# Optimization experiments

Measured on AMD Instinct MI355X. Metric: run time of the kernel, lower is better.

## Reference

```python
import jax, jax.numpy as jnp
import numpy as np

S, B, D = 2048, 4, 512
H, R, QK, FFN = 8, 8, 32, 2048
HD = D // H  # 64


def _ln(x, g, b, eps=1e-5):
    mu = jnp.mean(x, axis=-1, keepdims=True)
    var = jnp.var(x, axis=-1, keepdims=True)
    return (x - mu) * jax.lax.rsqrt(var + eps) * g + b


def setup_inputs() -> dict:
    key = jax.random.key(0)
    ks = jax.random.split(key, 16)
    w = lambda k, shape: (jax.random.normal(k, shape, jnp.float32) * 0.02)
    return {
        "x": jax.random.normal(ks[0], (S, B, D), jnp.float32),
        "Wq": w(ks[1], (D, D)),        "bq": jnp.zeros((D,), jnp.float32),
        "Wk": w(ks[2], (D, D)),        "bk": jnp.zeros((D,), jnp.float32),
        "Wv": w(ks[3], (D, HD * R)),   "bv": jnp.zeros((HD * R,), jnp.float32),
        "Wqv": w(ks[4], (D, QK * H)),  "bqv": jnp.zeros((QK * H,), jnp.float32),
        "Wkv": w(ks[5], (HD, QK)),     "bkv": jnp.zeros((QK,), jnp.float32),
        "Wf": w(ks[6], (D, D)),        "bf": jnp.zeros((D,), jnp.float32),
        "W1": w(ks[7], (D, FFN)),      "b1": jnp.zeros((FFN,), jnp.float32),
        "W2": w(ks[8], (FFN, D)),      "b2": jnp.zeros((D,), jnp.float32),
        "g1": jnp.ones((D,), jnp.float32),  "be1": jnp.zeros((D,), jnp.float32),
        "g2": jnp.ones((D,), jnp.float32),  "be2": jnp.zeros((D,), jnp.float32),
    }


def reference(x, Wq, bq, Wk, bk, Wv, bv, Wqv, bqv, Wkv, bkv, Wf, bf,
              W1, b1, W2, b2, g1, be1, g2, be2):
    # x: [S, B, D] -> [B, S, D]
    xb = jnp.transpose(x, (1, 0, 2))
    bsz, n, _ = xb.shape
    res = xb

    # stage 1: per-head attention over positions
    q = (xb @ Wq + bq).reshape(bsz, n, H, HD) / np.sqrt(HD).astype(np.float32)
    k = (xb @ Wk + bk).reshape(bsz, n, H, HD)
    v = (xb @ Wv + bv).reshape(bsz, n, R, HD)
    score = jax.nn.softmax(jnp.einsum("bshd,bthd->bhst", q, k), axis=-1)  # [B,H,S,S]
    # retrieved values per (head, rule): [B, S, H, R, HD]
    out = jnp.einsum("bhst,btrd->bshrd", score, v)

    # stage 2: composition softmax over rules
    qv = (xb @ Wqv + bqv).reshape(bsz, n, H, QK) / np.sqrt(QK).astype(np.float32)
    kv = out @ Wkv + bkv  # [B,S,H,R,QK]
    comp = jax.nn.softmax(jnp.einsum("bshq,bshrq->bshr", qv, kv), axis=-1)
    o = jnp.einsum("bshr,bshrd->bshd", comp, out).reshape(bsz, n, D)
    o = o @ Wf + bf

    # post-norm residual + FFN (norm_before=False)
    o = _ln(res + o, g1, be1)
    ffn = jax.nn.relu(o @ W1 + b1) @ W2 + b2
    o = _ln(o + ffn, g2, be2)
    return jnp.transpose(o, (1, 0, 2))  # back to [S, B, D]
```

## Files before the change

### kernel.cpp

```cpp
#include <hip/hip_runtime.h>
#include <hip/hip_bf16.h>

typedef __bf16 bf16;
typedef bf16 bf16x4 __attribute__((ext_vector_type(4)));
typedef bf16 bf16x8 __attribute__((ext_vector_type(8)));
typedef float f32x4 __attribute__((ext_vector_type(4)));

constexpr int SEQ  = 2048;
constexpr int BAT  = 4;
constexpr int NH   = 8;
constexpr int NTOK = SEQ * BAT;
constexpr int QKVW = 1792;
constexpr size_t MB = 1ull << 20;

__device__ inline void async_lds16(const void* g, void* l) {
  __builtin_amdgcn_global_load_lds(
      (__attribute__((address_space(1))) void*)(g),
      (__attribute__((address_space(3))) void*)(l), 16, 0, 0);
}

#define MFMA16 __builtin_amdgcn_mfma_f32_16x16x32_bf16

__global__ __launch_bounds__(512)
void attn_kernel(const bf16* __restrict__ qkv, const bf16* __restrict__ vT,
                 bf16* __restrict__ outb) {
  __shared__ __align__(16) bf16 Qs[64 * 64];
  __shared__ __align__(16) bf16 Ks[2][256 * 64];
  __shared__ __align__(16) bf16 Ps[2][64 * 128];
  __shared__ float rsAll[8][64];
  __shared__ float rsInv[64];

  const int tid = threadIdx.x;
  const int lane = tid & 63, w = tid >> 6;
  const int r16 = lane & 15, rq = lane >> 4;
  const int qb = blockIdx.x, h = blockIdx.y, b = blockIdx.z;

  const bf16* qbase = qkv + ((long)b * SEQ + qb * 64) * QKVW + h * 64;
  {
    const int rr = tid >> 3, sl = tid & 7;
    async_lds16(qbase + (long)rr * QKVW + ((sl ^ (rr & 7)) << 3),
                Qs + (size_t)w * 512);
  }
  const bf16* kbase = qkv + (long)b * SEQ * QKVW + 512 + h * 64;
  auto stageK = [&](int buf, int t0) {
#pragma unroll
    for (int g = 0; g < 4; g++) {
      const int c = g * 512 + tid;
      const int rr = c >> 3, sl = c & 7;
      async_lds16(kbase + (long)(t0 + rr) * QKVW + ((sl ^ (rr & 7)) << 3),
                  Ks[buf] + (size_t)(g * 8 + w) * 512);
    }
  };
  const bf16* vp[4];
#pragma unroll
  for (int n = 0; n < 4; n++)
    vp[n] = vT + ((long)b * 512 + w * 64 + n * 16 + r16) * SEQ + rq * 8;

  f32x4 acc[4][4] = {};
  float rs[4] = {};

  stageK(0, 0);
  asm volatile("s_waitcnt vmcnt(0)" ::: "memory");
  __builtin_amdgcn_s_barrier();
  __builtin_amdgcn_sched_barrier(0);

  bf16x8 qf[4][2];
#pragma unroll
  for (int j = 0; j < 4; j++)
#pragma unroll
    for (int kf = 0; kf < 2; kf++) {
      const int row = j * 16 + r16;
      qf[j][kf] = *(const bf16x8*)&Qs[row * 64 + (((kf * 4 + rq) ^ (row & 7)) << 3)];
    }

  const int krow = w * 16 + r16;
  for (int t = 0; t < 8; ++t) {
    const int t0 = t * 256;
    if (t) {
      asm volatile("s_waitcnt vmcnt(0)" ::: "memory");
      __builtin_amdgcn_s_barrier();
      __builtin_amdgcn_sched_barrier(0);
    }
    if (t < 7) stageK((t + 1) & 1, t0 + 256);
    bf16x8 vcur[4];
#pragma unroll
    for (int n = 0; n < 4; n++)
      vcur[n] = *(const bf16x8*)(vp[n] + t0);
    bf16x8 kfa[2], kfb[2];
#pragma unroll
    for (int kf = 0; kf < 2; kf++) {
      const int so = (((kf * 4 + rq) ^ (krow & 7)) << 3);
      kfa[kf] = *(const bf16x8*)&Ks[t & 1][krow * 64 + so];
      kfb[kf] = *(const bf16x8*)&Ks[t & 1][(128 + krow) * 64 + so];
    }
    f32x4 sA[4] = {}, sB[4] = {};
#pragma unroll
    for (int j = 0; j < 4; j++) {
      sA[j] = MFMA16(kfa[0], qf[j][0], sA[j], 0, 0, 0);
      sA[j] = MFMA16(kfa[1], qf[j][1], sA[j], 0, 0, 0);
      sB[j] = MFMA16(kfb[0], qf[j][0], sB[j], 0, 0, 0);
      sB[j] = MFMA16(kfb[1], qf[j][1], sB[j], 0, 0, 0);
    }
#pragma unroll
    for (int half = 0; half < 2; half++) {
      bf16* Pcur = Ps[half];
#pragma unroll
      for (int j = 0; j < 4; j++) {
        const f32x4 sv = half ? sB[j] : sA[j];
        const float e0 = __expf(sv[0]), e1 = __expf(sv[1]);
        const float e2 = __expf(sv[2]), e3 = __expf(sv[3]);
        rs[j] += (e0 + e1) + (e2 + e3);
        bf16x4 pk; pk[0] = (bf16)e0; pk[1] = (bf16)e1; pk[2] = (bf16)e2; pk[3] = (bf16)e3;
        const int row = j * 16 + r16;
        *(bf16x4*)&Pcur[row * 128 + (((w * 2 + (rq >> 1)) ^ (row & 7)) << 3) + ((rq & 1) << 2)] = pk;
      }
    }
    asm volatile("s_waitcnt lgkmcnt(0)" ::: "memory");
    __builtin_amdgcn_s_barrier();
    __builtin_amdgcn_sched_barrier(0);
#pragma unroll
    for (int g = 0; g < 8; g++) {
      const int half = g >> 2, c = g & 3;
      bf16x8 vnxt[4];
      if (g < 7) {
#pragma unroll
        for (int n = 0; n < 4; n++)
          vnxt[n] = *(const bf16x8*)(vp[n] + t0 + (g + 1) * 32);
      }
      bf16x8 pf[4];
#pragma unroll
      for (int i = 0; i < 4; i++) {
        const int row = i * 16 + r16;
        pf[i] = *(const bf16x8*)&Ps[half][row * 128 + (((rq + c * 4) ^ (row & 7)) << 3)];
      }
      __builtin_amdgcn_s_setprio(1);
#pragma unroll
      for (int i = 0; i < 4; i++) {
        acc[i][0] = MFMA16(pf[i], vcur[0], acc[i][0], 0, 0, 0);
        acc[i][1] = MFMA16(pf[i], vcur[1], acc[i][1], 0, 0, 0);
        acc[i][2] = MFMA16(pf[i], vcur[2], acc[i][2], 0, 0, 0);
        acc[i][3] = MFMA16(pf[i], vcur[3], acc[i][3], 0, 0, 0);
      }
      __builtin_amdgcn_s_setprio(0);
#pragma unroll
      for (int n = 0; n < 4; n++) vcur[n] = vnxt[n];
    }
    __builtin_amdgcn_s_barrier();
  }

#pragma unroll
  for (int j = 0; j < 4; j++) {
    rs[j] += __shfl_xor(rs[j], 16);
    rs[j] += __shfl_xor(rs[j], 32);
  }
  if (rq == 0) {
#pragma unroll
    for (int j = 0; j < 4; j++) rsAll[w][j * 16 + r16] = rs[j];
  }
  asm volatile("s_waitcnt lgkmcnt(0)" ::: "memory");
  __builtin_amdgcn_s_barrier();
  if (tid < 64) {
    float tot = 0.f;
#pragma unroll
    for (int u = 0; u < 8; u++) tot += rsAll[u][tid];
    rsInv[tid] = 1.f / tot;
  }
  asm volatile("s_waitcnt lgkmcnt(0)" ::: "memory");
  __builtin_amdgcn_s_barrier();

  bf16* obase = outb + (((long)(b * NH + h) * SEQ) + qb * 64) * 512 + w * 64;
#pragma unroll
  for (int i = 0; i < 4; i++) {
#pragma unroll
    for (int rg = 0; rg < 4; rg++) {
      const int row = i * 16 + rq * 4 + rg;
      const float inv = rsInv[row];
#pragma unroll
      for (int n = 0; n < 4; n++)
        obase[(long)row * 512 + n * 16 + r16] = (bf16)(acc[i][n][rg] * inv);
    }
  }
}

__global__ __launch_bounds__(256)
void gemm_bt(const bf16* __restrict__ A, const bf16* __restrict__ B,
             void* __restrict__ C, const float* __restrict__ bias,
             int K, int lda, int ldb, int ldc,
             long sAz, long sBz, long sCz,
             float scale, int flags) {
  constexpr int LPT = 4;
  __shared__ __align__(16) bf16 As[3][128 * 32];
  __shared__ __align__(16) bf16 Bs[3][128 * 32];

  const int tid  = threadIdx.x;
  const int lane = tid & 63;
  const int w    = tid >> 6;
  const int wr   = w >> 1, wc = w & 1;

  const int gx = gridDim.x, gy = gridDim.y;
  const int nwg = gx * gy * gridDim.z;
  const int flat = blockIdx.x + gx * (blockIdx.y + gy * blockIdx.z);
  const int q = nwg >> 3, r = nwg & 7;
  const int xcd = flat & 7, pos = flat >> 3;
  int swz = (xcd < r ? xcd * (q + 1) : r * (q + 1) + (xcd - r) * q) + pos;
  const int bx = swz % gx; swz /= gx;
  const int by = swz % gy;
  const long z = swz / gy;

  const bf16* Ab = A + (long)by * 128 * lda + z * sAz;
  const bf16* Bb = B + (long)bx * 128 * ldb + z * sBz;

  const bf16* aSrc[2];
  const bf16* bSrc[2];
#pragma unroll
  for (int g = 0; g < 2; g++) {
    const int c = (w * 2 + g) * 64 + lane;
    const int rr = c >> 2, sl = c & 3;
    aSrc[g] = Ab + (long)rr * lda + ((sl ^ ((rr >> 1) & 3)) << 3);
    bSrc[g] = Bb + (long)rr * ldb + ((sl ^ ((rr >> 1) & 3)) << 3);
  }

  f32x4 acc[4][4] = {};
  const int r16 = lane & 15, kq = lane >> 4;
  const int so = ((kq ^ ((r16 >> 1) & 3)) << 3);

  auto stage = [&](int buf, int k0) {
#pragma unroll
    for (int g = 0; g < 2; g++)
      async_lds16(aSrc[g] + k0, &As[buf][(w * 2 + g) * 512]);
#pragma unroll
    for (int g = 0; g < 2; g++)
      async_lds16(bSrc[g] + k0, &Bs[buf][(w * 2 + g) * 512]);
  };
  bf16x8 areg[4], breg[4];
  auto loadfrags = [&](int buf) {
#pragma unroll
    for (int i = 0; i < 4; i++)
      areg[i] = *(const bf16x8*)&As[buf][(wr * 64 + i * 16 + r16) * 32 + so];
#pragma unroll
    for (int j = 0; j < 4; j++)
      breg[j] = *(const bf16x8*)&Bs[buf][(wc * 64 + j * 16 + r16) * 32 + so];
  };
  auto domfma = [&]() {
    __builtin_amdgcn_s_setprio(1);
#pragma unroll
    for (int i = 0; i < 4; i++)
#pragma unroll
      for (int j = 0; j < 4; j++)
        acc[i][j] = MFMA16(areg[i], breg[j], acc[i][j], 0, 0, 0);
    __builtin_amdgcn_s_setprio(0);
  };

  const int nt = K >> 5;
  stage(0, 0);
  if (nt > 1) stage(1, 32);

  int cs = 2, cc = 0;
  for (int t = 0; t + 2 < nt; ++t) {
    stage(cs, (t + 2) * 32);
    asm volatile("s_waitcnt vmcnt(%0)" : : "n"(2 * LPT) : "memory");
    __builtin_amdgcn_s_barrier();
    loadfrags(cc);
    asm volatile("s_waitcnt lgkmcnt(0)" : : : "memory");
    __builtin_amdgcn_sched_barrier(0);
    __builtin_amdgcn_s_barrier();
    domfma();
    if (++cs == 3) cs = 0;
    if (++cc == 3) cc = 0;
  }
  if (nt >= 2) {
    asm volatile("s_waitcnt vmcnt(%0)" : : "n"(LPT) : "memory");
    __builtin_amdgcn_s_barrier();
    loadfrags(cc);
    asm volatile("s_waitcnt lgkmcnt(0)" : : : "memory");
    __builtin_amdgcn_sched_barrier(0);
    domfma();
    if (++cc == 3) cc = 0;
  }
  asm volatile("s_waitcnt vmcnt(0)" : : : "memory");
  __builtin_amdgcn_s_barrier();
  loadfrags(cc);
  domfma();

  const long rowBase = (long)by * 128 + wr * 64;
  const int  colBase = bx * 128 + wc * 64;
  float* Cf = (float*)C;
  bf16*  Cb = (bf16*)C;
  const int rq = lane >> 4;
#pragma unroll
  for (int i = 0; i < 4; i++) {
#pragma unroll
    for (int j = 0; j < 4; j++) {
      const int col = colBase + j * 16 + r16;
      const float bv = (bias && z == 0) ? bias[col] : 0.f;
#pragma unroll
      for (int rg = 0; rg < 4; rg++) {
        const long row = rowBase + i * 16 + rq * 4 + rg;
        float y = (acc[i][j][rg] + bv) * scale;
        if (flags & 2) y = fmaxf(y, 0.f);
        const long idx = z * sCz + row * (long)ldc + col;
        if (flags & 1) Cb[idx] = (bf16)y;
        else           Cf[idx] = y;
      }
    }
  }
}

__global__ void transpose_w_kernel(const float* __restrict__ in, bf16* __restrict__ out,
                                   int K, int N, float scale) {
  __shared__ float t[32][33];
  const int n0 = blockIdx.x * 32, k0 = blockIdx.y * 32;
  const int tx = threadIdx.x, ty = threadIdx.y;
#pragma unroll
  for (int i = ty; i < 32; i += 8)
    t[i][tx] = in[(long)(k0 + i) * N + n0 + tx];
  __syncthreads();
#pragma unroll
  for (int i = ty; i < 32; i += 8)
    out[(long)(n0 + i) * K + k0 + tx] = (bf16)(t[tx][i] * scale);
}

__global__ void build_bias_kernel(const float* bq, const float* bk,
                                  const float* bv, const float* bqv,
                                  float* __restrict__ out) {
  const int i = blockIdx.x * 256 + threadIdx.x;
  float v;
  if (i < 512)       v = bq[i] * 0.125f;
  else if (i < 1024) v = bk[i - 512];
  else if (i < 1536) v = bv[i - 1024];
  else               v = bqv[i - 1536] * 0.17677669529663687f;
  out[i] = v;
}

__global__ void transpose_v_kernel(const bf16* __restrict__ qkv, bf16* __restrict__ vT) {
  __shared__ bf16 t[32][33];
  const int s0 = blockIdx.x * 32, c0 = blockIdx.y * 32, b = blockIdx.z;
  const int tx = threadIdx.x, ty = threadIdx.y;
#pragma unroll
  for (int i = ty; i < 32; i += 8)
    t[i][tx] = qkv[((long)b * SEQ + s0 + i) * QKVW + 1024 + c0 + tx];
  __syncthreads();
#pragma unroll
  for (int i = ty; i < 32; i += 8)
    vT[(long)b * 512 * SEQ + (long)(c0 + i) * SEQ + s0 + tx] = t[tx][i];
}

__global__ __launch_bounds__(256)
void convert_x_kernel(const float* __restrict__ x, bf16* __restrict__ xb) {
  const long i0 = ((long)blockIdx.x * 256 + threadIdx.x) * 8;
  const int t = (int)(i0 >> 9), d = (int)(i0 & 511);
  const int b = t >> 11, s = t & 2047;
  const float* src = x + ((long)(s * BAT + b) << 9) + d;
  const float4 f0 = *(const float4*)(src);
  const float4 f1 = *(const float4*)(src + 4);
  bf16x8 o;
  o[0] = (bf16)f0.x; o[1] = (bf16)f0.y; o[2] = (bf16)f0.z; o[3] = (bf16)f0.w;
  o[4] = (bf16)f1.x; o[5] = (bf16)f1.y; o[6] = (bf16)f1.z; o[7] = (bf16)f1.w;
  *(bf16x8*)&xb[i0] = o;
}

__global__ __launch_bounds__(256)
void stage2_kernel(const bf16* __restrict__ outbuf, long strideB,
                   const bf16* __restrict__ qvb, int qvStride,
                   const float* __restrict__ Wkv,
                   const float* __restrict__ bkv,
                   bf16* __restrict__ attn) {
  const int lane = threadIdx.x & 63, wid = threadIdx.x >> 6;
  const int g = blockIdx.x * 4 + wid;
  const int s = g & 2047, h = (g >> 11) & 7, b = g >> 14;
  const int token = b * SEQ + s;

  const bf16* qv = qvb + (long)token * qvStride + h * 32;
  const float* wrow = Wkv + lane * 32;
  float wq = 0.f, cb = 0.f;
#pragma unroll 8
  for (int q = 0; q < 32; q++) {
    const float qf = (float)qv[q];
    wq += wrow[q] * qf;
    cb += bkv[q] * qf;
  }

  const bf16* orow = outbuf + b * strideB + ((long)(h << 11) + s) * 512;
  float of[8], lg[8];
#pragma unroll
  for (int r = 0; r < 8; r++) {
    of[r] = (float)orow[r * 64 + lane];
    float p = of[r] * wq;
    for (int o = 1; o < 64; o <<= 1) p += __shfl_xor(p, o);
    lg[r] = p + cb;
  }
  float m = lg[0];
#pragma unroll
  for (int r = 1; r < 8; r++) m = fmaxf(m, lg[r]);
  float e[8], sum = 0.f;
#pragma unroll
  for (int r = 0; r < 8; r++) { e[r] = __expf(lg[r] - m); sum += e[r]; }
  const float inv = 1.f / sum;
  float o = 0.f;
#pragma unroll
  for (int r = 0; r < 8; r++) o += e[r] * inv * of[r];
  attn[(long)token * 512 + h * 64 + lane] = (bf16)o;
}

__global__ __launch_bounds__(256)
void ln_kernel(const float* __restrict__ a, long part2,
               const float* __restrict__ bres, int bresT,
               const float* __restrict__ g, const float* __restrict__ be,
               float* __restrict__ outF, bf16* __restrict__ outB, int outT) {
  __shared__ float red[8];
  const int t = blockIdx.x, tid = threadIdx.x;
  const int b = t >> 11, s = t & 2047;
  const long ti = (long)t * 512;
  const long xi = (long)(s * BAT + b) * 512;
  const long ri = bresT ? xi : ti;
  float v0 = a[ti + tid]       + bres[ri + tid];
  float v1 = a[ti + 256 + tid] + bres[ri + 256 + tid];
  if (part2) { v0 += a[part2 + ti + tid]; v1 += a[part2 + ti + 256 + tid]; }
  float sum = v0 + v1, sq = v0 * v0 + v1 * v1;
  const int lane = tid & 63, wid = tid >> 6;
  for (int o = 1; o < 64; o <<= 1) { sum += __shfl_xor(sum, o); sq += __shfl_xor(sq, o); }
  if (lane == 0) { red[wid] = sum; red[4 + wid] = sq; }
  __syncthreads();
  sum = red[0] + red[1] + red[2] + red[3];
  sq  = red[4] + red[5] + red[6] + red[7];
  const float mu = sum * (1.f / 512.f);
  const float var = sq * (1.f / 512.f) - mu * mu;
  const float rs = rsqrtf(var + 1e-5f);
  const float y0 = (v0 - mu) * rs * g[tid] + be[tid];
  const float y1 = (v1 - mu) * rs * g[tid + 256] + be[tid + 256];
  const long oi = outT ? xi : ti;
  if (outF) { outF[oi + tid] = y0; outF[oi + 256 + tid] = y1; }
  if (outB) { outB[ti + tid] = (bf16)y0; outB[ti + 256 + tid] = (bf16)y1; }
}

extern "C" void kernel_launch(void* const* d_in, const int* in_sizes, int n_in,
                              void* d_out, int out_size, void* d_ws, size_t ws_size,
                              hipStream_t stream) {
  const float* x   = (const float*)d_in[0];
  const float* Wq  = (const float*)d_in[1];
  const float* bq  = (const float*)d_in[2];
  const float* Wk  = (const float*)d_in[3];
  const float* bk  = (const float*)d_in[4];
  const float* Wv  = (const float*)d_in[5];
  const float* bv  = (const float*)d_in[6];
  const float* Wqv = (const float*)d_in[7];
  const float* bqv = (const float*)d_in[8];
  const float* Wkv = (const float*)d_in[9];
  const float* bkv = (const float*)d_in[10];
  const float* Wf  = (const float*)d_in[11];
  const float* bfc = (const float*)d_in[12];
  const float* W1  = (const float*)d_in[13];
  const float* b1  = (const float*)d_in[14];
  const float* W2  = (const float*)d_in[15];
  const float* b2  = (const float*)d_in[16];
  const float* g1  = (const float*)d_in[17];
  const float* be1 = (const float*)d_in[18];
  const float* g2  = (const float*)d_in[19];
  const float* be2 = (const float*)d_in[20];

  char* ws = (char*)d_ws;
  size_t off = 0;
  auto alloc = [&](size_t bytes) -> void* {
    void* p = ws + off;
    off += (bytes + 1023) & ~(size_t)1023;
    return p;
  };
  bf16*  qkv   = (bf16*)alloc((size_t)NTOK * QKVW * 2);
  bf16*  vT    = (bf16*)alloc((size_t)BAT * 512 * SEQ * 2);
  bf16*  wtPk  = (bf16*)alloc((size_t)QKVW * 512 * 2);
  bf16*  WfT   = (bf16*)alloc(512 * 512 * 2);
  bf16*  W1T   = (bf16*)alloc((size_t)2048 * 512 * 2);
  bf16*  W2T   = (bf16*)alloc((size_t)512 * 2048 * 2);
  float* bcat  = (float*)alloc(QKVW * 4);
  bf16*  attn  = (bf16*)alloc((size_t)NTOK * 512 * 2);

  char* reg = ws + off;
  bf16*  outb  = (bf16*)reg;
  bf16*  xb    = (bf16*)reg;
  float* wfoP  = (float*)(reg + 8 * MB);
  float* ln1f  = (float*)(reg + 40 * MB);
  bf16*  ln1b  = (bf16*)(reg + 56 * MB);
  bf16*  ffn1  = (bf16*)(reg + 64 * MB);

  const dim3 tb(32, 8);
  transpose_w_kernel<<<dim3(16, 16), tb, 0, stream>>>(Wq,  wtPk,              512, 512, 0.125f);
  transpose_w_kernel<<<dim3(16, 16), tb, 0, stream>>>(Wk,  wtPk + 512  * 512, 512, 512, 1.f);
  transpose_w_kernel<<<dim3(16, 16), tb, 0, stream>>>(Wv,  wtPk + 1024 * 512, 512, 512, 1.f);
  transpose_w_kernel<<<dim3(8, 16),  tb, 0, stream>>>(Wqv, wtPk + 1536 * 512, 512, 256, 0.17677669529663687f);
  transpose_w_kernel<<<dim3(16, 16), tb, 0, stream>>>(Wf,  WfT, 512, 512, 1.f);
  transpose_w_kernel<<<dim3(64, 16), tb, 0, stream>>>(W1,  W1T, 512, 2048, 1.f);
  transpose_w_kernel<<<dim3(16, 64), tb, 0, stream>>>(W2,  W2T, 2048, 512, 1.f);
  build_bias_kernel<<<7, 256, 0, stream>>>(bq, bk, bv, bqv, bcat);
  convert_x_kernel<<<2048, 256, 0, stream>>>(x, xb);

  gemm_bt<<<dim3(14, 64, 1), 256, 0, stream>>>(xb, wtPk, qkv, bcat,
      512, 512, 512, QKVW, 0, 0, 0, 1.f, 1);

  transpose_v_kernel<<<dim3(64, 16, 4), tb, 0, stream>>>(qkv, vT);

  attn_kernel<<<dim3(SEQ / 64, NH, BAT), 512, 0, stream>>>(qkv, vT, outb);

  stage2_kernel<<<BAT * NH * SEQ / 4, 256, 0, stream>>>(outb, (long)NH * SEQ * 512,
      qkv + 1536, QKVW, Wkv, bkv, attn);

  const long sWf = (long)NTOK * 512;
  gemm_bt<<<dim3(4, 64, 2), 256, 0, stream>>>(attn, WfT, wfoP, bfc,
      256, 512, 512, 512, 256, 256, sWf, 1.f, 0);
  ln_kernel<<<NTOK, 256, 0, stream>>>(wfoP, sWf, x, 1, g1, be1, ln1f, ln1b, 0);
  gemm_bt<<<dim3(16, 64, 1), 256, 0, stream>>>(ln1b, W1T, ffn1, b1,
      512, 512, 512, 2048, 0, 0, 0, 1.f, 1 | 2);
  gemm_bt<<<dim3(4, 64, 2), 256, 0, stream>>>(ffn1, W2T, wfoP, b2,
      1024, 2048, 2048, 512, 1024, 1024, sWf, 1.f, 0);
  ln_kernel<<<NTOK, 256, 0, stream>>>(wfoP, sWf, ln1f, 0, g2, be2, (float*)d_out, nullptr, 1);
}
```

Baseline: 521.4 us.

## Deepen V prefetch to two stages, pad P tile, and swizzle block order

The attention kernel now keeps two V fragments in flight instead of one, issuing them before the K staging so global latency is better hidden behind the PV MFMAs. The P LDS tile row stride is padded from 128 to 136 elements to change the bank mapping. The block index is remapped so that consecutive workgroups are spread across heads and batches, which is meant to improve L2 locality and spread load across XCDs. The deeper prefetch costs extra VGPRs, and the padding combined with the existing XOR swizzle may not reduce bank conflicts.

```diff
diff --git a/kernel.cpp b/kernel.cpp
--- a/kernel.cpp
+++ b/kernel.cpp
@@ -21,19 +21,24 @@
 
 #define MFMA16 __builtin_amdgcn_mfma_f32_16x16x32_bf16
 
+constexpr int PLD = 136;
+
 __global__ __launch_bounds__(512)
 void attn_kernel(const bf16* __restrict__ qkv, const bf16* __restrict__ vT,
                  bf16* __restrict__ outb) {
   __shared__ __align__(16) bf16 Qs[64 * 64];
   __shared__ __align__(16) bf16 Ks[2][256 * 64];
-  __shared__ __align__(16) bf16 Ps[2][64 * 128];
+  __shared__ __align__(16) bf16 Ps[2][64 * PLD];
   __shared__ float rsAll[8][64];
   __shared__ float rsInv[64];
 
   const int tid = threadIdx.x;
   const int lane = tid & 63, w = tid >> 6;
   const int r16 = lane & 15, rq = lane >> 4;
-  const int qb = blockIdx.x, h = blockIdx.y, b = blockIdx.z;
+
+  const int flat = blockIdx.x + 32 * (blockIdx.y + 8 * blockIdx.z);
+  const int swz = (flat & 7) * 128 + (flat >> 3);
+  const int qb = swz & 31, h = (swz >> 5) & 7, b = swz >> 8;
 
   const bf16* qbase = qkv + ((long)b * SEQ + qb * 64) * QKVW + h * 64;
   {
@@ -81,11 +86,14 @@
       __builtin_amdgcn_s_barrier();
       __builtin_amdgcn_sched_barrier(0);
     }
+    bf16x8 v0[4], v1[4];
+#pragma unroll
+    for (int n = 0; n < 4; n++) v0[n] = *(const bf16x8*)(vp[n] + t0);
+#pragma unroll
+    for (int n = 0; n < 4; n++) v1[n] = *(const bf16x8*)(vp[n] + t0 + 32);
+    __builtin_amdgcn_sched_barrier(0);
     if (t < 7) stageK((t + 1) & 1, t0 + 256);
-    bf16x8 vcur[4];
-#pragma unroll
-    for (int n = 0; n < 4; n++)
-      vcur[n] = *(const bf16x8*)(vp[n] + t0);
+    __builtin_amdgcn_sched_barrier(0);
     bf16x8 kfa[2], kfb[2];
 #pragma unroll
     for (int kf = 0; kf < 2; kf++) {
@@ -112,7 +120,7 @@
         rs[j] += (e0 + e1) + (e2 + e3);
         bf16x4 pk; pk[0] = (bf16)e0; pk[1] = (bf16)e1; pk[2] = (bf16)e2; pk[3] = (bf16)e3;
         const int row = j * 16 + r16;
-        *(bf16x4*)&Pcur[row * 128 + (((w * 2 + (rq >> 1)) ^ (row & 7)) << 3) + ((rq & 1) << 2)] = pk;
+        *(bf16x4*)&Pcur[row * PLD + (((w * 2 + (rq >> 1)) ^ (row & 7)) << 3) + ((rq & 1) << 2)] = pk;
       }
     }
     asm volatile("s_waitcnt lgkmcnt(0)" ::: "memory");
@@ -121,29 +129,29 @@
 #pragma unroll
     for (int g = 0; g < 8; g++) {
       const int half = g >> 2, c = g & 3;
-      bf16x8 vnxt[4];
-      if (g < 7) {
+      bf16x8 v2[4];
+      if (g < 6) {
 #pragma unroll
         for (int n = 0; n < 4; n++)
-          vnxt[n] = *(const bf16x8*)(vp[n] + t0 + (g + 1) * 32);
+          v2[n] = *(const bf16x8*)(vp[n] + t0 + (g + 2) * 32);
       }
       bf16x8 pf[4];
 #pragma unroll
       for (int i = 0; i < 4; i++) {
         const int row = i * 16 + r16;
-        pf[i] = *(const bf16x8*)&Ps[half][row * 128 + (((rq + c * 4) ^ (row & 7)) << 3)];
+        pf[i] = *(const bf16x8*)&Ps[half][row * PLD + (((rq + c * 4) ^ (row & 7)) << 3)];
       }
       __builtin_amdgcn_s_setprio(1);
 #pragma unroll
       for (int i = 0; i < 4; i++) {
-        acc[i][0] = MFMA16(pf[i], vcur[0], acc[i][0], 0, 0, 0);
-        acc[i][1] = MFMA16(pf[i], vcur[1], acc[i][1], 0, 0, 0);
-        acc[i][2] = MFMA16(pf[i], vcur[2], acc[i][2], 0, 0, 0);
-        acc[i][3] = MFMA16(pf[i], vcur[3], acc[i][3], 0, 0, 0);
+        acc[i][0] = MFMA16(pf[i], v0[0], acc[i][0], 0, 0, 0);
+        acc[i][1] = MFMA16(pf[i], v0[1], acc[i][1], 0, 0, 0);
+        acc[i][2] = MFMA16(pf[i], v0[2], acc[i][2], 0, 0, 0);
+        acc[i][3] = MFMA16(pf[i], v0[3], acc[i][3], 0, 0, 0);
       }
       __builtin_amdgcn_s_setprio(0);
 #pragma unroll
-      for (int n = 0; n < 4; n++) vcur[n] = vnxt[n];
+      for (int n = 0; n < 4; n++) { v0[n] = v1[n]; v1[n] = v2[n]; }
     }
     __builtin_amdgcn_s_barrier();
   }
```

Result: no change. 520.4 us (-0.2%).

## Fuse rule-composition stage into attention kernel epilogue, use exp2 softmax

Applied to the files above, without the earlier changes.

The composition softmax over rules moves into the attention kernel's epilogue. The big per-head, per-rule output tensor (B*H*S*512 bf16) is no longer written to global memory and read back by a separate stage2 kernel. The epilogue folds Wkv into the query (qv·Wkv^T), reduces logits across waves through LDS, applies the softmax over the 8 rules, and sums the weighted rule outputs through an LDS slab. Separately, the score scale now includes log2(e) so exp2f can replace __expf. The epilogue adds several block barriers and LDS traffic, and the rule outputs are rounded to bf16 before the sum, which may change numerics slightly.

```diff
diff --git a/kernel.cpp b/kernel.cpp
--- a/kernel.cpp
+++ b/kernel.cpp
@@ -23,12 +23,19 @@
 
 __global__ __launch_bounds__(512)
 void attn_kernel(const bf16* __restrict__ qkv, const bf16* __restrict__ vT,
-                 bf16* __restrict__ outb) {
-  __shared__ __align__(16) bf16 Qs[64 * 64];
-  __shared__ __align__(16) bf16 Ks[2][256 * 64];
-  __shared__ __align__(16) bf16 Ps[2][64 * 128];
+                 const float* __restrict__ Wkv, const float* __restrict__ bkv,
+                 bf16* __restrict__ attnOut) {
+  __shared__ __align__(16) char MAIN[8192 + 2 * 32768 + 2 * 16384];
+  bf16* Qs  = (bf16*)MAIN;
+  bf16* Ks0 = (bf16*)(MAIN + 8192);
+  bf16* Ks1 = (bf16*)(MAIN + 8192 + 32768);
+  bf16* Ps0 = (bf16*)(MAIN + 73728);
+  bf16* Ps1 = (bf16*)(MAIN + 73728 + 16384);
   __shared__ float rsAll[8][64];
   __shared__ float rsInv[64];
+  __shared__ float cbL[64];
+  __shared__ float lgL[8][64];
+  __shared__ float cpL[8][64];
 
   const int tid = threadIdx.x;
   const int lane = tid & 63, w = tid >> 6;
@@ -42,13 +49,13 @@
                 Qs + (size_t)w * 512);
   }
   const bf16* kbase = qkv + (long)b * SEQ * QKVW + 512 + h * 64;
-  auto stageK = [&](int buf, int t0) {
+  auto stageK = [&](bf16* dst, int t0) {
 #pragma unroll
     for (int g = 0; g < 4; g++) {
       const int c = g * 512 + tid;
       const int rr = c >> 3, sl = c & 7;
       async_lds16(kbase + (long)(t0 + rr) * QKVW + ((sl ^ (rr & 7)) << 3),
-                  Ks[buf] + (size_t)(g * 8 + w) * 512);
+                  dst + (size_t)(g * 8 + w) * 512);
     }
   };
   const bf16* vp[4];
@@ -59,7 +66,7 @@
   f32x4 acc[4][4] = {};
   float rs[4] = {};
 
-  stageK(0, 0);
+  stageK(Ks0, 0);
   asm volatile("s_waitcnt vmcnt(0)" ::: "memory");
   __builtin_amdgcn_s_barrier();
   __builtin_amdgcn_sched_barrier(0);
@@ -76,12 +83,14 @@
   const int krow = w * 16 + r16;
   for (int t = 0; t < 8; ++t) {
     const int t0 = t * 256;
+    const bf16* Kc = (t & 1) ? Ks1 : Ks0;
+    bf16* Kn = (t & 1) ? Ks0 : Ks1;
     if (t) {
       asm volatile("s_waitcnt vmcnt(0)" ::: "memory");
       __builtin_amdgcn_s_barrier();
       __builtin_amdgcn_sched_barrier(0);
     }
-    if (t < 7) stageK((t + 1) & 1, t0 + 256);
+    if (t < 7) stageK(Kn, t0 + 256);
     bf16x8 vcur[4];
 #pragma unroll
     for (int n = 0; n < 4; n++)
@@ -90,8 +99,8 @@
 #pragma unroll
     for (int kf = 0; kf < 2; kf++) {
       const int so = (((kf * 4 + rq) ^ (krow & 7)) << 3);
-      kfa[kf] = *(const bf16x8*)&Ks[t & 1][krow * 64 + so];
-      kfb[kf] = *(const bf16x8*)&Ks[t & 1][(128 + krow) * 64 + so];
+      kfa[kf] = *(const bf16x8*)&Kc[krow * 64 + so];
+      kfb[kf] = *(const bf16x8*)&Kc[(128 + krow) * 64 + so];
     }
     f32x4 sA[4] = {}, sB[4] = {};
 #pragma unroll
@@ -103,12 +112,12 @@
     }
 #pragma unroll
     for (int half = 0; half < 2; half++) {
-      bf16* Pcur = Ps[half];
+      bf16* Pcur = half ? Ps1 : Ps0;
 #pragma unroll
       for (int j = 0; j < 4; j++) {
         const f32x4 sv = half ? sB[j] : sA[j];
-        const float e0 = __expf(sv[0]), e1 = __expf(sv[1]);
-        const float e2 = __expf(sv[2]), e3 = __expf(sv[3]);
+        const float e0 = exp2f(sv[0]), e1 = exp2f(sv[1]);
+        const float e2 = exp2f(sv[2]), e3 = exp2f(sv[3]);
         rs[j] += (e0 + e1) + (e2 + e3);
         bf16x4 pk; pk[0] = (bf16)e0; pk[1] = (bf16)e1; pk[2] = (bf16)e2; pk[3] = (bf16)e3;
         const int row = j * 16 + r16;
@@ -120,7 +129,8 @@
     __builtin_amdgcn_sched_barrier(0);
 #pragma unroll
     for (int g = 0; g < 8; g++) {
-      const int half = g >> 2, c = g & 3;
+      const bf16* Ph = (g >> 2) ? Ps1 : Ps0;
+      const int c = g & 3;
       bf16x8 vnxt[4];
       if (g < 7) {
 #pragma unroll
@@ -131,7 +141,7 @@
 #pragma unroll
       for (int i = 0; i < 4; i++) {
         const int row = i * 16 + r16;
-        pf[i] = *(const bf16x8*)&Ps[half][row * 128 + (((rq + c * 4) ^ (row & 7)) << 3)];
+        pf[i] = *(const bf16x8*)&Ph[row * 128 + (((rq + c * 4) ^ (row & 7)) << 3)];
       }
       __builtin_amdgcn_s_setprio(1);
 #pragma unroll
@@ -157,28 +167,104 @@
 #pragma unroll
     for (int j = 0; j < 4; j++) rsAll[w][j * 16 + r16] = rs[j];
   }
-  asm volatile("s_waitcnt lgkmcnt(0)" ::: "memory");
-  __builtin_amdgcn_s_barrier();
+  __syncthreads();
   if (tid < 64) {
     float tot = 0.f;
 #pragma unroll
     for (int u = 0; u < 8; u++) tot += rsAll[u][tid];
     rsInv[tid] = 1.f / tot;
   }
-  asm volatile("s_waitcnt lgkmcnt(0)" ::: "memory");
-  __builtin_amdgcn_s_barrier();
-
-  bf16* obase = outb + (((long)(b * NH + h) * SEQ) + qb * 64) * 512 + w * 64;
+  __syncthreads();
+
+  bf16*  qvL   = (bf16*)MAIN;
+  float* WkvL  = (float*)(MAIN + 8192);
+  float* wqL   = (float*)(MAIN + 16384);
+  bf16*  slab  = (bf16*)(MAIN + 32768);
+
+  {
+    const int qrow = tid >> 3, q0 = (tid & 7) * 4;
+    *(bf16x4*)&qvL[qrow * 32 + q0] =
+        *(const bf16x4*)(qkv + ((long)(b * SEQ + qb * 64 + qrow)) * QKVW + 1536 + h * 32 + q0);
+    *(float4*)&WkvL[tid * 4] = *(const float4*)&Wkv[tid * 4];
+  }
+  __syncthreads();
+  {
+    const int qrow = tid & 63, hd0 = (tid >> 6) * 8;
+    float s[8] = {};
+#pragma unroll 4
+    for (int q = 0; q < 32; q++) {
+      const float qf = (float)qvL[qrow * 32 + q];
+#pragma unroll
+      for (int d = 0; d < 8; d++) s[d] += WkvL[(hd0 + d) * 32 + q] * qf;
+    }
+#pragma unroll
+    for (int d = 0; d < 8; d++) wqL[qrow * 64 + hd0 + d] = s[d];
+    if (tid < 64) {
+      float cs = 0.f;
+      for (int q = 0; q < 32; q++) cs += bkv[q] * (float)qvL[tid * 32 + q];
+      cbL[tid] = cs;
+    }
+  }
+  __syncthreads();
 #pragma unroll
   for (int i = 0; i < 4; i++) {
 #pragma unroll
     for (int rg = 0; rg < 4; rg++) {
-      const int row = i * 16 + rq * 4 + rg;
-      const float inv = rsInv[row];
+      const int qrow = i * 16 + rq * 4 + rg;
+      float p = 0.f;
 #pragma unroll
       for (int n = 0; n < 4; n++)
-        obase[(long)row * 512 + n * 16 + r16] = (bf16)(acc[i][n][rg] * inv);
-    }
+        p += acc[i][n][rg] * wqL[qrow * 64 + n * 16 + r16];
+      p *= rsInv[qrow];
+      p += __shfl_xor(p, 1); p += __shfl_xor(p, 2);
+      p += __shfl_xor(p, 4); p += __shfl_xor(p, 8);
+      if (r16 == 0) lgL[w][qrow] = p + cbL[qrow];
+    }
+  }
+  __syncthreads();
+  if (tid < 64) {
+    float l[8];
+#pragma unroll
+    for (int r = 0; r < 8; r++) l[r] = lgL[r][tid];
+    float m = l[0];
+#pragma unroll
+    for (int r = 1; r < 8; r++) m = fmaxf(m, l[r]);
+    float e[8], sum = 0.f;
+#pragma unroll
+    for (int r = 0; r < 8; r++) { e[r] = __expf(l[r] - m); sum += e[r]; }
+    const float inv = 1.f / sum;
+#pragma unroll
+    for (int r = 0; r < 8; r++) cpL[r][tid] = e[r] * inv;
+  }
+  __syncthreads();
+  {
+    bf16* ms = slab + w * 4096;
+#pragma unroll
+    for (int i = 0; i < 4; i++) {
+#pragma unroll
+      for (int rg = 0; rg < 4; rg++) {
+        const int qrow = i * 16 + rq * 4 + rg;
+        const float cw = cpL[w][qrow] * rsInv[qrow];
+#pragma unroll
+        for (int n = 0; n < 4; n++)
+          ms[qrow * 64 + n * 16 + r16] = (bf16)(acc[i][n][rg] * cw);
+      }
+    }
+  }
+  __syncthreads();
+  {
+    const int qrow = tid >> 3, hd0 = (tid & 7) * 8;
+    float o[8] = {};
+#pragma unroll
+    for (int r = 0; r < 8; r++) {
+      const bf16x8 v = *(const bf16x8*)&slab[r * 4096 + qrow * 64 + hd0];
+#pragma unroll
+      for (int e = 0; e < 8; e++) o[e] += (float)v[e];
+    }
+    bf16x8 ov;
+#pragma unroll
+    for (int e = 0; e < 8; e++) ov[e] = (bf16)o[e];
+    *(bf16x8*)&attnOut[((long)(b * SEQ + qb * 64 + qrow)) * 512 + h * 64 + hd0] = ov;
   }
 }
 
@@ -325,7 +411,7 @@
                                   float* __restrict__ out) {
   const int i = blockIdx.x * 256 + threadIdx.x;
   float v;
-  if (i < 512)       v = bq[i] * 0.125f;
+  if (i < 512)       v = bq[i] * 0.18033688011112042f;
   else if (i < 1024) v = bk[i - 512];
   else if (i < 1536) v = bv[i - 1024];
   else               v = bqv[i - 1536] * 0.17677669529663687f;
@@ -357,49 +443,6 @@
   o[0] = (bf16)f0.x; o[1] = (bf16)f0.y; o[2] = (bf16)f0.z; o[3] = (bf16)f0.w;
   o[4] = (bf16)f1.x; o[5] = (bf16)f1.y; o[6] = (bf16)f1.z; o[7] = (bf16)f1.w;
   *(bf16x8*)&xb[i0] = o;
-}
-
-__global__ __launch_bounds__(256)
-void stage2_kernel(const bf16* __restrict__ outbuf, long strideB,
-                   const bf16* __restrict__ qvb, int qvStride,
-                   const float* __restrict__ Wkv,
-                   const float* __restrict__ bkv,
-                   bf16* __restrict__ attn) {
-  const int lane = threadIdx.x & 63, wid = threadIdx.x >> 6;
-  const int g = blockIdx.x * 4 + wid;
-  const int s = g & 2047, h = (g >> 11) & 7, b = g >> 14;
-  const int token = b * SEQ + s;
-
-  const bf16* qv = qvb + (long)token * qvStride + h * 32;
-  const float* wrow = Wkv + lane * 32;
-  float wq = 0.f, cb = 0.f;
-#pragma unroll 8
-  for (int q = 0; q < 32; q++) {
-    const float qf = (float)qv[q];
-    wq += wrow[q] * qf;
-    cb += bkv[q] * qf;
-  }
-
-  const bf16* orow = outbuf + b * strideB + ((long)(h << 11) + s) * 512;
-  float of[8], lg[8];
-#pragma unroll
-  for (int r = 0; r < 8; r++) {
-    of[r] = (float)orow[r * 64 + lane];
-    float p = of[r] * wq;
-    for (int o = 1; o < 64; o <<= 1) p += __shfl_xor(p, o);
-    lg[r] = p + cb;
-  }
-  float m = lg[0];
-#pragma unroll
-  for (int r = 1; r < 8; r++) m = fmaxf(m, lg[r]);
-  float e[8], sum = 0.f;
-#pragma unroll
-  for (int r = 0; r < 8; r++) { e[r] = __expf(lg[r] - m); sum += e[r]; }
-  const float inv = 1.f / sum;
-  float o = 0.f;
-#pragma unroll
-  for (int r = 0; r < 8; r++) o += e[r] * inv * of[r];
-  attn[(long)token * 512 + h * 64 + lane] = (bf16)o;
 }
 
 __global__ __launch_bounds__(256)
@@ -475,7 +518,6 @@
   bf16*  attn  = (bf16*)alloc((size_t)NTOK * 512 * 2);
 
   char* reg = ws + off;
-  bf16*  outb  = (bf16*)reg;
   bf16*  xb    = (bf16*)reg;
   float* wfoP  = (float*)(reg + 8 * MB);
   float* ln1f  = (float*)(reg + 40 * MB);
@@ -483,7 +525,7 @@
   bf16*  ffn1  = (bf16*)(reg + 64 * MB);
 
   const dim3 tb(32, 8);
-  transpose_w_kernel<<<dim3(16, 16), tb, 0, stream>>>(Wq,  wtPk,              512, 512, 0.125f);
+  transpose_w_kernel<<<dim3(16, 16), tb, 0, stream>>>(Wq,  wtPk,              512, 512, 0.18033688011112042f);
   transpose_w_kernel<<<dim3(16, 16), tb, 0, stream>>>(Wk,  wtPk + 512  * 512, 512, 512, 1.f);
   transpose_w_kernel<<<dim3(16, 16), tb, 0, stream>>>(Wv,  wtPk + 1024 * 512, 512, 512, 1.f);
   transpose_w_kernel<<<dim3(8, 16),  tb, 0, stream>>>(Wqv, wtPk + 1536 * 512, 512, 256, 0.17677669529663687f);
@@ -498,10 +540,7 @@
 
   transpose_v_kernel<<<dim3(64, 16, 4), tb, 0, stream>>>(qkv, vT);
 
-  attn_kernel<<<dim3(SEQ / 64, NH, BAT), 512, 0, stream>>>(qkv, vT, outb);
-
-  stage2_kernel<<<BAT * NH * SEQ / 4, 256, 0, stream>>>(outb, (long)NH * SEQ * 512,
-      qkv + 1536, QKVW, Wkv, bkv, attn);
+  attn_kernel<<<dim3(SEQ / 64, NH, BAT), 512, 0, stream>>>(qkv, vT, Wkv, bkv, attn);
 
   const long sWf = (long)NTOK * 512;
   gemm_bt<<<dim3(4, 64, 2), 256, 0, stream>>>(attn, WfT, wfoP, bfc,
```

After: 468.0 us. 10.3% less time.
